# Kernel optimization log

Measured on AMD Instinct MI355X. Metric: run time of the kernel, lower is better.

The kernel has to match this reference:

```python
import jax, jax.numpy as jnp
import numpy as np

B, T, C, H = 2, 64, 384, 768
LR, MOM, DECAY = 0.01, 0.9, 0.001


def pscan(gates, tokens):
    """parallel_scan_log: x[t] = gates[t]*x[t-1] + tokens[t] along axis 1.
    gates [B,S], tokens [B,S,...]."""
    extra = tokens.ndim - gates.ndim
    g = gates.reshape(gates.shape + (1,) * extra)
    g = jnp.clip(g, 1e-7, 1.0 - 1e-7)
    lc = jnp.cumsum(jnp.log(g), axis=1)              # log cumulative gates
    return jnp.exp(lc) * jnp.cumsum(tokens * jnp.exp(-lc), axis=1)


def setup_inputs():
    key = jax.random.key(0)
    ks = jax.random.split(key, 12)
    s = 0.02
    W0 = jax.random.normal(ks[0], (H, C), jnp.float32) * s
    W1 = jax.random.normal(ks[1], (C, H), jnp.float32) * s
    return {
        "x": jax.random.normal(ks[2], (B, T, C), jnp.float32),
        "Wq": jax.random.normal(ks[3], (C, C), jnp.float32) * s, "bq": jnp.zeros((C,), jnp.float32),
        "Wk": jax.random.normal(ks[4], (C, C), jnp.float32) * s, "bk": jnp.zeros((C,), jnp.float32),
        "Wv": jax.random.normal(ks[5], (C, C), jnp.float32) * s, "bv": jnp.zeros((C,), jnp.float32),
        "Wo": jax.random.normal(ks[6], (C, C), jnp.float32) * s, "bo": jnp.zeros((C,), jnp.float32),
        "init_query": jax.random.normal(ks[7], (1, 1, C), jnp.float32) * s,
        "sW0": jnp.broadcast_to(W0, (B, H, C)) + 0.0,
        "sb0": jnp.zeros((B, H), jnp.float32),
        "sW1": jnp.broadcast_to(W1, (B, C, H)) + 0.0,
        "sb1": jnp.zeros((B, C), jnp.float32),
    }


def reference(x, Wq, bq, Wk, bk, Wv, bv, Wo, bo, init_query, sW0, sb0, sW1, sb1):
    dt = x.dtype
    # ---- retrieval (causal: uses init_query since no previous segment) ----
    q = jnp.broadcast_to(init_query, (B, 1, C)) @ Wq.T + bq          # [B,1,C]
    h_pre = jnp.einsum('bqc,bhc->bqh', q, sW0) + sb0[:, None]
    h = h_pre * jax.nn.sigmoid(h_pre)                                 # SiLU
    pred = jnp.einsum('bqh,bch->bqc', h, sW1) + sb1[:, None]
    out = pred @ Wo.T + bo                                            # [B,1,C]

    # ---- test-time memory update: per-token MSE gradients ----
    k = x @ Wk.T + bk                                                 # [B,T,C]
    v = x @ Wv.T + bv
    h1_pre = jnp.einsum('btc,bhc->bth', k, sW0) + sb0[:, None]
    sig = jax.nn.sigmoid(h1_pre)
    h1 = h1_pre * sig
    p = jnp.einsum('bth,bch->btc', h1, sW1) + sb1[:, None]
    dp = p - v                                                        # d(MSE)/d(pred)
    dW1 = jnp.einsum('btc,bth->btch', dp, h1)                         # [B,T,C,H]
    db1 = dp
    dh1 = jnp.einsum('btc,bch->bth', dp, sW1)
    dh1p = dh1 * (sig * (1 + h1_pre * (1 - sig)))                     # SiLU grad
    dW0 = jnp.einsum('bth,btc->bthc', dh1p, k)                        # [B,T,H,C]
    db0 = dh1p

    # ---- momentum scan + decayed weight scan ----
    def update(W, g):
        surprise = -LR * g                                            # [B,T,...]
        m = pscan(jnp.full((B, T), MOM, dt), (1.0 - MOM) * surprise)  # EMA of surprises
        toks = jnp.concatenate([W[:, None], m], axis=1)               # seed with current weight
        gts = jnp.concatenate([jnp.ones((B, 1), dt),
                               jnp.full((B, T), 1.0 - DECAY, dt)], axis=1)
        return pscan(gts, toks)[:, -1]                                # final weight after segment

    nW0 = update(sW0, dW0)
    nb0 = update(sb0, db0)
    nW1 = update(sW1, dW1)
    nb1 = update(sb1, db1)
    return out, nW0, nb0, nW1, nb1
```

## Files before the change

### kernel.cpp

```cpp
#include <hip/hip_runtime.h>
#include <hip/hip_bf16.h>
#include <cmath>

#define BB 2
#define TT 64
#define CC 384
#define HH 768

#define O_OUT 0
#define O_NW0 768
#define O_NB0 (768 + 589824)
#define O_NW1 (O_NB0 + 1536)
#define O_NB1 (O_NW1 + 589824)

struct Coefs { float ct[TT]; float dfac; };

typedef __attribute__((ext_vector_type(8))) short bf16x8;
typedef __attribute__((ext_vector_type(4))) float f32x4;

__device__ __forceinline__ float bf2f(unsigned short u) {
    union { unsigned int i; float f; } x; x.i = ((unsigned int)u) << 16; return x.f;
}
__device__ __forceinline__ unsigned short f2bf(float f) {
    union { float f; unsigned int i; } u; u.f = f;
    unsigned int x = u.i;
    unsigned int r = (x + 0x7fffu + ((x >> 16) & 1u)) >> 16;
    return (unsigned short)r;
}
__device__ __forceinline__ f32x4 mfma16(bf16x8 a, bf16x8 b, f32x4 c) {
    return __builtin_amdgcn_mfma_f32_16x16x32_bf16(a, b, c, 0, 0, 0);
}
__device__ __forceinline__ bf16x8 ldbf8(const unsigned short* p) {
    return *(const bf16x8*)p;
}

__global__ void k_conv(const float* __restrict__ x,  const float* __restrict__ Wq,
                       const float* __restrict__ Wk, const float* __restrict__ Wv,
                       const float* __restrict__ Wo, const float* __restrict__ sW0,
                       const float* __restrict__ sW1,
                       unsigned short* __restrict__ x_bf,  unsigned short* __restrict__ Wq_bf,
                       unsigned short* __restrict__ Wk_bf, unsigned short* __restrict__ Wv_bf,
                       unsigned short* __restrict__ Wo_bf, unsigned short* __restrict__ sW0_bf,
                       unsigned short* __restrict__ sW1_bf, unsigned short* __restrict__ sW1T_bf) {
    const int blk = blockIdx.x, j = threadIdx.x;
    if (blk < 1776) {
        int g = blk * 256 + j;
        const float* src; unsigned short* dst; int off;
        if      (g < 12288)  { src = x;   dst = x_bf;   off = g; }
        else if (g < 49152)  { src = Wq;  dst = Wq_bf;  off = g - 12288; }
        else if (g < 86016)  { src = Wk;  dst = Wk_bf;  off = g - 49152; }
        else if (g < 122880) { src = Wv;  dst = Wv_bf;  off = g - 86016; }
        else if (g < 159744) { src = Wo;  dst = Wo_bf;  off = g - 122880; }
        else if (g < 307200) { src = sW0; dst = sW0_bf; off = g - 159744; }
        else                 { src = sW1; dst = sW1_bf; off = g - 307200; }
        float4 v = ((const float4*)src)[off];
        ushort4 u;
        u.x = f2bf(v.x); u.y = f2bf(v.y); u.z = f2bf(v.z); u.w = f2bf(v.w);
        ((ushort4*)dst)[off] = u;
    } else {
        __shared__ float tile[32][33];
        const int r2 = blk - 1776;
        const int b = r2 / 288, rem = r2 % 288;
        const int c0 = (rem / 24) * 32, h0 = (rem % 24) * 32;
        const int row0 = j / 32, col = j % 32;
        #pragma unroll
        for (int r = 0; r < 4; ++r) {
            int row = row0 + r * 8;
            tile[row][col] = sW1[((size_t)(b * CC + c0 + row)) * HH + h0 + col];
        }
        __syncthreads();
        #pragma unroll
        for (int r = 0; r < 4; ++r) {
            int row = row0 + r * 8;
            sW1T_bf[((size_t)(b * HH + h0 + row)) * CC + c0 + col] = f2bf(tile[col][row]);
        }
    }
}

__global__ void k_qkv(const unsigned short* __restrict__ x_bf,
                      const unsigned short* __restrict__ Wk_bf, const float* __restrict__ bk,
                      const unsigned short* __restrict__ Wv_bf, const float* __restrict__ bv,
                      const unsigned short* __restrict__ Wq_bf, const float* __restrict__ bq,
                      const float* __restrict__ iq,
                      unsigned short* __restrict__ kb_bf, float* __restrict__ vb,
                      float* __restrict__ qb) {
    __shared__ float vecs[CC];
    __shared__ float part[16][17];
    const int blk = blockIdx.x, j = threadIdx.x;
    if (blk < 24) {
        const int wid = j >> 6, L = j & 63;
        const int w = blk * 4 + wid;
        const int mp = w % 4, np = w / 4;
        const int lrow = L & 15, kq = (L >> 4) * 8;
        const unsigned short* A0 = x_bf + (size_t)(mp * 32 + lrow) * CC;
        const unsigned short* A1 = A0 + 16 * CC;
        const int n0 = (2 * np) * 16 + lrow, n1 = n0 + 16;
        const unsigned short* B0 = (n0 < CC) ? (Wk_bf + (size_t)n0 * CC) : (Wv_bf + (size_t)(n0 - CC) * CC);
        const unsigned short* B1 = (n1 < CC) ? (Wk_bf + (size_t)n1 * CC) : (Wv_bf + (size_t)(n1 - CC) * CC);
        f32x4 acc00 = {0,0,0,0}, acc01 = {0,0,0,0}, acc10 = {0,0,0,0}, acc11 = {0,0,0,0};
        for (int s = 0; s < CC / 32; ++s) {
            int k = s * 32 + kq;
            bf16x8 a0 = ldbf8(A0 + k), a1 = ldbf8(A1 + k);
            bf16x8 b0 = ldbf8(B0 + k), b1 = ldbf8(B1 + k);
            acc00 = mfma16(a0, b0, acc00); acc01 = mfma16(a0, b1, acc01);
            acc10 = mfma16(a1, b0, acc10); acc11 = mfma16(a1, b1, acc11);
        }
        const int quad = L >> 4;
        #pragma unroll
        for (int mi = 0; mi < 2; ++mi) {
            #pragma unroll
            for (int ni = 0; ni < 2; ++ni) {
                f32x4 acc = mi == 0 ? (ni == 0 ? acc00 : acc01) : (ni == 0 ? acc10 : acc11);
                int n = (2 * np + ni) * 16 + lrow;
                #pragma unroll
                for (int r = 0; r < 4; ++r) {
                    int m = mp * 32 + mi * 16 + quad * 4 + r;
                    float v = acc[r];
                    if (n < CC) kb_bf[(size_t)m * CC + n] = f2bf(v + bk[n]);
                    else        vb[(size_t)m * CC + (n - CC)] = v + bv[n - CC];
                }
            }
        }
    } else {
        if (j < CC / 4) ((float4*)vecs)[j] = ((const float4*)iq)[j];
        __syncthreads();
        const int nt = blk - 24;
        const int nl = j & 15, ks = j >> 4;
        const int n = nt * 16 + nl;
        const unsigned short* wr = Wq_bf + (size_t)n * CC + ks * 24;
        float s = 0.f;
        for (int i = 0; i < 3; ++i) {
            bf16x8 wv8 = ldbf8(wr + i * 8);
            #pragma unroll
            for (int e = 0; e < 8; ++e)
                s += bf2f((unsigned short)wv8[e]) * vecs[ks * 24 + i * 8 + e];
        }
        part[ks][nl] = s;
        __syncthreads();
        if (j < 16) {
            float acc = bq[nt * 16 + j];
            #pragma unroll
            for (int kk = 0; kk < 16; ++kk) acc += part[kk][j];
            qb[nt * 16 + j] = acc;
        }
    }
}

__global__ void k_h1(const unsigned short* __restrict__ kb_bf, const float* __restrict__ qb,
                     const unsigned short* __restrict__ sW0_bf, const float* __restrict__ sb0,
                     unsigned short* __restrict__ h1_bf, float* __restrict__ dsil,
                     float* __restrict__ hret) {
    __shared__ float vecs[CC];
    __shared__ float part[16][17];
    const int blk = blockIdx.x, j = threadIdx.x;
    if (blk < 24) {
        const int b = blk / 12;
        const int wid = j >> 6, L = j & 63;
        const int w = (blk % 12) * 4 + wid;
        const int mp = w & 1, np = w >> 1;
        const int lrow = L & 15, kq = (L >> 4) * 8;
        const unsigned short* A0 = kb_bf + (size_t)(b * TT + mp * 32 + lrow) * CC;
        const unsigned short* A1 = A0 + 16 * CC;
        const int n0 = (2 * np) * 16 + lrow;
        const unsigned short* B0 = sW0_bf + (size_t)(b * HH + n0) * CC;
        const unsigned short* B1 = B0 + 16 * CC;
        f32x4 acc00 = {0,0,0,0}, acc01 = {0,0,0,0}, acc10 = {0,0,0,0}, acc11 = {0,0,0,0};
        for (int s = 0; s < CC / 32; ++s) {
            int k = s * 32 + kq;
            bf16x8 a0 = ldbf8(A0 + k), a1 = ldbf8(A1 + k);
            bf16x8 b0 = ldbf8(B0 + k), b1 = ldbf8(B1 + k);
            acc00 = mfma16(a0, b0, acc00); acc01 = mfma16(a0, b1, acc01);
            acc10 = mfma16(a1, b0, acc10); acc11 = mfma16(a1, b1, acc11);
        }
        const int quad = L >> 4;
        #pragma unroll
        for (int mi = 0; mi < 2; ++mi) {
            #pragma unroll
            for (int ni = 0; ni < 2; ++ni) {
                f32x4 acc = mi == 0 ? (ni == 0 ? acc00 : acc01) : (ni == 0 ? acc10 : acc11);
                int n = (2 * np + ni) * 16 + lrow;
                float bias = sb0[b * HH + n];
                #pragma unroll
                for (int r = 0; r < 4; ++r) {
                    int t = mp * 32 + mi * 16 + quad * 4 + r;
                    float pre = acc[r] + bias;
                    float sig = 1.f / (1.f + expf(-pre));
                    size_t idx = (size_t)(b * TT + t) * HH + n;
                    h1_bf[idx] = f2bf(pre * sig);
                    dsil[idx]  = sig * (1.f + pre * (1.f - sig));
                }
            }
        }
    } else {
        if (j < CC / 4) ((float4*)vecs)[j] = ((const float4*)qb)[j];
        __syncthreads();
        const int rb = blk - 24;
        const int b = rb / 48, nt = rb % 48;
        const int nl = j & 15, ks = j >> 4;
        const int n = nt * 16 + nl;
        const unsigned short* wr = sW0_bf + (size_t)(b * HH + n) * CC + ks * 24;
        float s = 0.f;
        for (int i = 0; i < 3; ++i) {
            bf16x8 wv8 = ldbf8(wr + i * 8);
            #pragma unroll
            for (int e = 0; e < 8; ++e)
                s += bf2f((unsigned short)wv8[e]) * vecs[ks * 24 + i * 8 + e];
        }
        part[ks][nl] = s;
        __syncthreads();
        if (j < 16) {
            int n2 = nt * 16 + j;
            float pre = sb0[b * HH + n2];
            #pragma unroll
            for (int kk = 0; kk < 16; ++kk) pre += part[kk][j];
            float sig = 1.f / (1.f + expf(-pre));
            hret[b * HH + n2] = pre * sig;
        }
    }
}

__global__ void k_p(const unsigned short* __restrict__ h1_bf, const float* __restrict__ hret,
                    const float* __restrict__ vb,
                    const unsigned short* __restrict__ sW1_bf, const float* __restrict__ sb1,
                    unsigned short* __restrict__ dp_bf, float* __restrict__ pred) {
    __shared__ float vecs[HH];
    __shared__ float part[16][17];
    const int blk = blockIdx.x, j = threadIdx.x;
    if (blk < 12) {
        const int b = blk / 6;
        const int wid = j >> 6, L = j & 63;
        const int w = (blk % 6) * 4 + wid;
        const int mp = w & 1, np = w >> 1;
        const int lrow = L & 15, kq = (L >> 4) * 8;
        const unsigned short* A0 = h1_bf + (size_t)(b * TT + mp * 32 + lrow) * HH;
        const unsigned short* A1 = A0 + 16 * HH;
        const int n0 = (2 * np) * 16 + lrow;
        const unsigned short* B0 = sW1_bf + (size_t)(b * CC + n0) * HH;
        const unsigned short* B1 = B0 + 16 * HH;
        f32x4 acc00 = {0,0,0,0}, acc01 = {0,0,0,0}, acc10 = {0,0,0,0}, acc11 = {0,0,0,0};
        for (int s = 0; s < HH / 32; ++s) {
            int k = s * 32 + kq;
            bf16x8 a0 = ldbf8(A0 + k), a1 = ldbf8(A1 + k);
            bf16x8 b0 = ldbf8(B0 + k), b1 = ldbf8(B1 + k);
            acc00 = mfma16(a0, b0, acc00); acc01 = mfma16(a0, b1, acc01);
            acc10 = mfma16(a1, b0, acc10); acc11 = mfma16(a1, b1, acc11);
        }
        const int quad = L >> 4;
        #pragma unroll
        for (int mi = 0; mi < 2; ++mi) {
            #pragma unroll
            for (int ni = 0; ni < 2; ++ni) {
                f32x4 acc = mi == 0 ? (ni == 0 ? acc00 : acc01) : (ni == 0 ? acc10 : acc11);
                int n = (2 * np + ni) * 16 + lrow;
                float bias = sb1[b * CC + n];
                #pragma unroll
                for (int r = 0; r < 4; ++r) {
                    int t = mp * 32 + mi * 16 + quad * 4 + r;
                    size_t idx = (size_t)(b * TT + t) * CC + n;
                    dp_bf[idx] = f2bf(acc[r] + bias - vb[idx]);
                }
            }
        }
    } else {
        const int rb = blk - 12;
        const int b = rb / 24, nt = rb % 24;
        if (j < HH / 4) ((float4*)vecs)[j] = ((const float4*)(hret + b * HH))[j];
        __syncthreads();
        const int nl = j & 15, ks = j >> 4;
        const int n = nt * 16 + nl;
        const unsigned short* wr = sW1_bf + (size_t)(b * CC + n) * HH + ks * 48;
        float s = 0.f;
        for (int i = 0; i < 6; ++i) {
            bf16x8 wv8 = ldbf8(wr + i * 8);
            #pragma unroll
            for (int e = 0; e < 8; ++e)
                s += bf2f((unsigned short)wv8[e]) * vecs[ks * 48 + i * 8 + e];
        }
        part[ks][nl] = s;
        __syncthreads();
        if (j < 16) {
            int n2 = nt * 16 + j;
            float acc = sb1[b * CC + n2];
            #pragma unroll
            for (int kk = 0; kk < 16; ++kk) acc += part[kk][j];
            pred[b * CC + n2] = acc;
        }
    }
}

__global__ void k_dh1(const unsigned short* __restrict__ dp_bf,
                      const unsigned short* __restrict__ sW1T_bf,
                      const float* __restrict__ dsil,
                      unsigned short* __restrict__ dh1p_bf) {
    const int blk = blockIdx.x, j = threadIdx.x;
    const int b = blk / 12;
    const int wid = j >> 6, L = j & 63;
    const int w = (blk % 12) * 4 + wid;
    const int mp = w & 1, np = w >> 1;
    const int lrow = L & 15, kq = (L >> 4) * 8;
    const unsigned short* A0 = dp_bf + (size_t)(b * TT + mp * 32 + lrow) * CC;
    const unsigned short* A1 = A0 + 16 * CC;
    const int n0 = (2 * np) * 16 + lrow;
    const unsigned short* B0 = sW1T_bf + (size_t)(b * HH + n0) * CC;
    const unsigned short* B1 = B0 + 16 * CC;
    f32x4 acc00 = {0,0,0,0}, acc01 = {0,0,0,0}, acc10 = {0,0,0,0}, acc11 = {0,0,0,0};
    for (int s = 0; s < CC / 32; ++s) {
        int k = s * 32 + kq;
        bf16x8 a0 = ldbf8(A0 + k), a1 = ldbf8(A1 + k);
        bf16x8 b0 = ldbf8(B0 + k), b1 = ldbf8(B1 + k);
        acc00 = mfma16(a0, b0, acc00); acc01 = mfma16(a0, b1, acc01);
        acc10 = mfma16(a1, b0, acc10); acc11 = mfma16(a1, b1, acc11);
    }
    const int quad = L >> 4;
    #pragma unroll
    for (int mi = 0; mi < 2; ++mi) {
        #pragma unroll
        for (int ni = 0; ni < 2; ++ni) {
            f32x4 acc = mi == 0 ? (ni == 0 ? acc00 : acc01) : (ni == 0 ? acc10 : acc11);
            int n = (2 * np + ni) * 16 + lrow;
            #pragma unroll
            for (int r = 0; r < 4; ++r) {
                int t = mp * 32 + mi * 16 + quad * 4 + r;
                size_t idx = (size_t)(b * TT + t) * HH + n;
                dh1p_bf[idx] = f2bf(acc[r] * dsil[idx]);
            }
        }
    }
}

__global__ void k_epi(const unsigned short* __restrict__ dp_bf,
                      const unsigned short* __restrict__ h1_bf,
                      const unsigned short* __restrict__ dh1p_bf,
                      const unsigned short* __restrict__ kb_bf,
                      const float* __restrict__ pred,
                      const float* __restrict__ sW0, const float* __restrict__ sb0,
                      const float* __restrict__ sW1, const float* __restrict__ sb1,
                      const unsigned short* __restrict__ Wo_bf, const float* __restrict__ bo,
                      float* __restrict__ out, Coefs cf) {
    __shared__ float a_t[TT][32];
    __shared__ float e_t[TT][64];
    __shared__ float vecs[CC];
    __shared__ float part[16][17];
    const int blk = blockIdx.x, j = threadIdx.x;

    if (blk < 288) {
        const int b = blk / 144, rem = blk % 144;
        const int c0 = (rem / 12) * 32, h0 = (rem % 12) * 64;
        for (int i = j; i < TT * 32; i += 256) {
            int t = i >> 5, c = i & 31;
            a_t[t][c] = cf.ct[t] * bf2f(dp_bf[((size_t)(b * TT + t)) * CC + c0 + c]);
        }
        for (int i = j; i < TT * 64; i += 256) {
            int t = i >> 6, h = i & 63;
            e_t[t][h] = bf2f(h1_bf[((size_t)(b * TT + t)) * HH + h0 + h]);
        }
        __syncthreads();
        const int ci = j & 31, hb = (j >> 5) * 8;
        float acc[8] = {0, 0, 0, 0, 0, 0, 0, 0};
        for (int t = 0; t < TT; ++t) {
            float av = a_t[t][ci];
            #pragma unroll
            for (int m = 0; m < 8; ++m) acc[m] += av * e_t[t][hb + m];
        }
        const size_t idx = ((size_t)b * CC + c0 + ci) * HH + h0 + hb;
        const float4* w4 = (const float4*)(sW1 + idx);
        float4 wa = w4[0], wb = w4[1];
        float4 o0, o1;
        o0.x = cf.dfac * wa.x - acc[0]; o0.y = cf.dfac * wa.y - acc[1];
        o0.z = cf.dfac * wa.z - acc[2]; o0.w = cf.dfac * wa.w - acc[3];
        o1.x = cf.dfac * wb.x - acc[4]; o1.y = cf.dfac * wb.y - acc[5];
        o1.z = cf.dfac * wb.z - acc[6]; o1.w = cf.dfac * wb.w - acc[7];
        *(float4*)(out + O_NW1 + idx) = o0;
        *(float4*)(out + O_NW1 + idx + 4) = o1;
    } else if (blk < 576) {
        const int bk2 = blk - 288;
        const int b = bk2 / 144, rem = bk2 % 144;
        const int h0 = (rem / 6) * 32, c0 = (rem % 6) * 64;
        for (int i = j; i < TT * 32; i += 256) {
            int t = i >> 5, h = i & 31;
            a_t[t][h] = cf.ct[t] * bf2f(dh1p_bf[((size_t)(b * TT + t)) * HH + h0 + h]);
        }
        for (int i = j; i < TT * 64; i += 256) {
            int t = i >> 6, c = i & 63;
            e_t[t][c] = bf2f(kb_bf[((size_t)(b * TT + t)) * CC + c0 + c]);
        }
        __syncthreads();
        const int hi = j & 31, cb = (j >> 5) * 8;
        float acc[8] = {0, 0, 0, 0, 0, 0, 0, 0};
        for (int t = 0; t < TT; ++t) {
            float av = a_t[t][hi];
            #pragma unroll
            for (int m = 0; m < 8; ++m) acc[m] += av * e_t[t][cb + m];
        }
        const size_t idx = ((size_t)b * HH + h0 + hi) * CC + c0 + cb;
        const float4* w4 = (const float4*)(sW0 + idx);
        float4 wa = w4[0], wb = w4[1];
        float4 o0, o1;
        o0.x = cf.dfac * wa.x - acc[0]; o0.y = cf.dfac * wa.y - acc[1];
        o0.z = cf.dfac * wa.z - acc[2]; o0.w = cf.dfac * wa.w - acc[3];
        o1.x = cf.dfac * wb.x - acc[4]; o1.y = cf.dfac * wb.y - acc[5];
        o1.z = cf.dfac * wb.z - acc[6]; o1.w = cf.dfac * wb.w - acc[7];
        *(float4*)(out + O_NW0 + idx) = o0;
        *(float4*)(out + O_NW0 + idx + 4) = o1;
    } else if (blk < 624) {
        const int rb = blk - 576;
        const int b = rb / 24, nt = rb % 24;
        if (j < CC / 4) ((float4*)vecs)[j] = ((const float4*)(pred + b * CC))[j];
        __syncthreads();
        const int nl = j & 15, ks = j >> 4;
        const int n = nt * 16 + nl;
        const unsigned short* wr = Wo_bf + (size_t)n * CC + ks * 24;
        float s = 0.f;
        for (int i = 0; i < 3; ++i) {
            bf16x8 wv8 = ldbf8(wr + i * 8);
            #pragma unroll
            for (int e = 0; e < 8; ++e)
                s += bf2f((unsigned short)wv8[e]) * vecs[ks * 24 + i * 8 + e];
        }
        part[ks][nl] = s;
        __syncthreads();
        if (j < 16) {
            int n2 = nt * 16 + j;
            float acc = bo[n2];
            #pragma unroll
            for (int kk = 0; kk < 16; ++kk) acc += part[kk][j];
            out[O_OUT + b * CC + n2] = acc;
        }
    } else {
        const int b = blk - 624;
        for (int c = j; c < CC; c += 256) {
            float acc = 0.f;
            for (int t = 0; t < TT; ++t)
                acc += cf.ct[t] * bf2f(dp_bf[((size_t)(b * TT + t)) * CC + c]);
            out[O_NB1 + b * CC + c] = cf.dfac * sb1[b * CC + c] - acc;
        }
        for (int h = j; h < HH; h += 256) {
            float acc = 0.f;
            for (int t = 0; t < TT; ++t)
                acc += cf.ct[t] * bf2f(dh1p_bf[((size_t)(b * TT + t)) * HH + h]);
            out[O_NB0 + b * HH + h] = cf.dfac * sb0[b * HH + h] - acc;
        }
    }
}

extern "C" void kernel_launch(void* const* d_in, const int* in_sizes, int n_in,
                              void* d_out, int out_size, void* d_ws, size_t ws_size,
                              hipStream_t stream) {
    const float* x   = (const float*)d_in[0];
    const float* Wq  = (const float*)d_in[1];
    const float* bq  = (const float*)d_in[2];
    const float* Wk  = (const float*)d_in[3];
    const float* bk  = (const float*)d_in[4];
    const float* Wv  = (const float*)d_in[5];
    const float* bv  = (const float*)d_in[6];
    const float* Wo  = (const float*)d_in[7];
    const float* bo  = (const float*)d_in[8];
    const float* iq  = (const float*)d_in[9];
    const float* sW0 = (const float*)d_in[10];
    const float* sb0 = (const float*)d_in[11];
    const float* sW1 = (const float*)d_in[12];
    const float* sb1 = (const float*)d_in[13];

    float* fw = (float*)d_ws;
    float* qb   = fw;
    float* hret = qb + 384;
    float* pred = hret + 1536;
    float* vb   = pred + 768;
    float* dsil = vb + 49152;
    unsigned short* us = (unsigned short*)(dsil + 98304);
    unsigned short* x_bf    = us;
    unsigned short* kb_bf   = x_bf + 49152;
    unsigned short* h1_bf   = kb_bf + 49152;
    unsigned short* dp_bf   = h1_bf + 98304;
    unsigned short* dh1p_bf = dp_bf + 49152;
    unsigned short* Wq_bf   = dh1p_bf + 98304;
    unsigned short* Wk_bf   = Wq_bf + 147456;
    unsigned short* Wv_bf   = Wk_bf + 147456;
    unsigned short* Wo_bf   = Wv_bf + 147456;
    unsigned short* sW0_bf  = Wo_bf + 147456;
    unsigned short* sW1_bf  = sW0_bf + 589824;
    unsigned short* sW1T_bf = sW1_bf + 589824;

    Coefs cf;
    const double mom = 0.9, decay = 1.0 - 0.001, lr = 0.01;
    for (int s = 0; s < TT; ++s) {
        double sum = 0.0;
        for (int t = s; t < TT; ++t) sum += pow(decay, (double)(TT - 1 - t)) * pow(mom, (double)(t - s));
        cf.ct[s] = (float)(lr * (1.0 - mom) * sum);
    }
    cf.dfac = (float)pow(decay, (double)TT);

    k_conv<<<dim3(1776 + 576), dim3(256), 0, stream>>>(x, Wq, Wk, Wv, Wo, sW0, sW1,
        x_bf, Wq_bf, Wk_bf, Wv_bf, Wo_bf, sW0_bf, sW1_bf, sW1T_bf);
    k_qkv<<<dim3(48), dim3(256), 0, stream>>>(x_bf, Wk_bf, bk, Wv_bf, bv, Wq_bf, bq, iq,
                                              kb_bf, vb, qb);
    k_h1 <<<dim3(120), dim3(256), 0, stream>>>(kb_bf, qb, sW0_bf, sb0, h1_bf, dsil, hret);
    k_p  <<<dim3(60), dim3(256), 0, stream>>>(h1_bf, hret, vb, sW1_bf, sb1, dp_bf, pred);
    k_dh1<<<dim3(24), dim3(256), 0, stream>>>(dp_bf, sW1T_bf, dsil, dh1p_bf);
    k_epi<<<dim3(626), dim3(256), 0, stream>>>(dp_bf, h1_bf, dh1p_bf, kb_bf, pred,
                                               sW0, sb0, sW1, sb1, Wo_bf, bo,
                                               (float*)d_out, cf);
}
```

Measured before the change: 144.6 us.

## Drop bf16 pre-conversion pass; convert fp32 operands inline and restructure epilogue kernels

Removes the standalone conversion kernel that wrote bf16 copies of all weights, including a transposed sW1. Each GEMM now loads fp32 operands directly and converts them to bf16 in registers, and the matrix-vector paths use fp32 weights. The dh1 GEMM reads sW1 with strided column loads instead of a pre-transposed copy, and is merged with the dW1, bias and output-projection work into k_epi1. The dW0 update moves to its own kernel, and the bias reductions are folded into the tile epilogues. This cuts a full pass over several MB of weights and one launch, at the cost of fp32 operand loads in the GEMMs and uncoalesced strided loads for the sW1 transpose path.

Result: no change. 145.8 us (+0.8%).

```diff
diff --git a/kernel.cpp b/kernel.cpp
--- a/kernel.cpp
+++ b/kernel.cpp
@@ -33,75 +33,45 @@
 __device__ __forceinline__ bf16x8 ldbf8(const unsigned short* p) {
     return *(const bf16x8*)p;
 }
-
-__global__ void k_conv(const float* __restrict__ x,  const float* __restrict__ Wq,
-                       const float* __restrict__ Wk, const float* __restrict__ Wv,
-                       const float* __restrict__ Wo, const float* __restrict__ sW0,
-                       const float* __restrict__ sW1,
-                       unsigned short* __restrict__ x_bf,  unsigned short* __restrict__ Wq_bf,
-                       unsigned short* __restrict__ Wk_bf, unsigned short* __restrict__ Wv_bf,
-                       unsigned short* __restrict__ Wo_bf, unsigned short* __restrict__ sW0_bf,
-                       unsigned short* __restrict__ sW1_bf, unsigned short* __restrict__ sW1T_bf) {
-    const int blk = blockIdx.x, j = threadIdx.x;
-    if (blk < 1776) {
-        int g = blk * 256 + j;
-        const float* src; unsigned short* dst; int off;
-        if      (g < 12288)  { src = x;   dst = x_bf;   off = g; }
-        else if (g < 49152)  { src = Wq;  dst = Wq_bf;  off = g - 12288; }
-        else if (g < 86016)  { src = Wk;  dst = Wk_bf;  off = g - 49152; }
-        else if (g < 122880) { src = Wv;  dst = Wv_bf;  off = g - 86016; }
-        else if (g < 159744) { src = Wo;  dst = Wo_bf;  off = g - 122880; }
-        else if (g < 307200) { src = sW0; dst = sW0_bf; off = g - 159744; }
-        else                 { src = sW1; dst = sW1_bf; off = g - 307200; }
-        float4 v = ((const float4*)src)[off];
-        ushort4 u;
-        u.x = f2bf(v.x); u.y = f2bf(v.y); u.z = f2bf(v.z); u.w = f2bf(v.w);
-        ((ushort4*)dst)[off] = u;
-    } else {
-        __shared__ float tile[32][33];
-        const int r2 = blk - 1776;
-        const int b = r2 / 288, rem = r2 % 288;
-        const int c0 = (rem / 24) * 32, h0 = (rem % 24) * 32;
-        const int row0 = j / 32, col = j % 32;
-        #pragma unroll
-        for (int r = 0; r < 4; ++r) {
-            int row = row0 + r * 8;
-            tile[row][col] = sW1[((size_t)(b * CC + c0 + row)) * HH + h0 + col];
-        }
-        __syncthreads();
-        #pragma unroll
-        for (int r = 0; r < 4; ++r) {
-            int row = row0 + r * 8;
-            sW1T_bf[((size_t)(b * HH + h0 + row)) * CC + c0 + col] = f2bf(tile[col][row]);
-        }
-    }
-}
-
-__global__ void k_qkv(const unsigned short* __restrict__ x_bf,
-                      const unsigned short* __restrict__ Wk_bf, const float* __restrict__ bk,
-                      const unsigned short* __restrict__ Wv_bf, const float* __restrict__ bv,
-                      const unsigned short* __restrict__ Wq_bf, const float* __restrict__ bq,
+__device__ __forceinline__ bf16x8 ldcvt8(const float* p) {
+    float4 a = *(const float4*)p, b = *(const float4*)(p + 4);
+    bf16x8 r;
+    r[0] = (short)f2bf(a.x); r[1] = (short)f2bf(a.y); r[2] = (short)f2bf(a.z); r[3] = (short)f2bf(a.w);
+    r[4] = (short)f2bf(b.x); r[5] = (short)f2bf(b.y); r[6] = (short)f2bf(b.z); r[7] = (short)f2bf(b.w);
+    return r;
+}
+__device__ __forceinline__ bf16x8 ldcvt8s(const float* p, int stride) {
+    bf16x8 r;
+    #pragma unroll
+    for (int i = 0; i < 8; ++i) r[i] = (short)f2bf(p[(size_t)i * stride]);
+    return r;
+}
+
+__global__ void k_qkv(const float* __restrict__ x,
+                      const float* __restrict__ Wk, const float* __restrict__ bk,
+                      const float* __restrict__ Wv, const float* __restrict__ bv,
+                      const float* __restrict__ Wq, const float* __restrict__ bq,
                       const float* __restrict__ iq,
                       unsigned short* __restrict__ kb_bf, float* __restrict__ vb,
                       float* __restrict__ qb) {
-    __shared__ float vecs[CC];
-    __shared__ float part[16][17];
+    __shared__ float smem[1024 + 16 * 17];
     const int blk = blockIdx.x, j = threadIdx.x;
     if (blk < 24) {
         const int wid = j >> 6, L = j & 63;
         const int w = blk * 4 + wid;
         const int mp = w % 4, np = w / 4;
         const int lrow = L & 15, kq = (L >> 4) * 8;
-        const unsigned short* A0 = x_bf + (size_t)(mp * 32 + lrow) * CC;
-        const unsigned short* A1 = A0 + 16 * CC;
+        const float* A0 = x + (size_t)(mp * 32 + lrow) * CC;
+        const float* A1 = A0 + 16 * CC;
         const int n0 = (2 * np) * 16 + lrow, n1 = n0 + 16;
-        const unsigned short* B0 = (n0 < CC) ? (Wk_bf + (size_t)n0 * CC) : (Wv_bf + (size_t)(n0 - CC) * CC);
-        const unsigned short* B1 = (n1 < CC) ? (Wk_bf + (size_t)n1 * CC) : (Wv_bf + (size_t)(n1 - CC) * CC);
+        const float* B0 = (n0 < CC) ? (Wk + (size_t)n0 * CC) : (Wv + (size_t)(n0 - CC) * CC);
+        const float* B1 = (n1 < CC) ? (Wk + (size_t)n1 * CC) : (Wv + (size_t)(n1 - CC) * CC);
         f32x4 acc00 = {0,0,0,0}, acc01 = {0,0,0,0}, acc10 = {0,0,0,0}, acc11 = {0,0,0,0};
+        #pragma unroll 2
         for (int s = 0; s < CC / 32; ++s) {
             int k = s * 32 + kq;
-            bf16x8 a0 = ldbf8(A0 + k), a1 = ldbf8(A1 + k);
-            bf16x8 b0 = ldbf8(B0 + k), b1 = ldbf8(B1 + k);
+            bf16x8 a0 = ldcvt8(A0 + k), a1 = ldcvt8(A1 + k);
+            bf16x8 b0 = ldcvt8(B0 + k), b1 = ldcvt8(B1 + k);
             acc00 = mfma16(a0, b0, acc00); acc01 = mfma16(a0, b1, acc01);
             acc10 = mfma16(a1, b0, acc10); acc11 = mfma16(a1, b1, acc11);
         }
@@ -122,36 +92,35 @@
             }
         }
     } else {
-        if (j < CC / 4) ((float4*)vecs)[j] = ((const float4*)iq)[j];
+        if (j < CC / 4) ((float4*)smem)[j] = ((const float4*)iq)[j];
         __syncthreads();
         const int nt = blk - 24;
         const int nl = j & 15, ks = j >> 4;
         const int n = nt * 16 + nl;
-        const unsigned short* wr = Wq_bf + (size_t)n * CC + ks * 24;
+        const float4* wr = (const float4*)(Wq + (size_t)n * CC + ks * 24);
         float s = 0.f;
-        for (int i = 0; i < 3; ++i) {
-            bf16x8 wv8 = ldbf8(wr + i * 8);
-            #pragma unroll
-            for (int e = 0; e < 8; ++e)
-                s += bf2f((unsigned short)wv8[e]) * vecs[ks * 24 + i * 8 + e];
-        }
-        part[ks][nl] = s;
+        #pragma unroll
+        for (int i = 0; i < 6; ++i) {
+            float4 a = wr[i];
+            const float* v = smem + ks * 24 + i * 4;
+            s += a.x * v[0] + a.y * v[1] + a.z * v[2] + a.w * v[3];
+        }
+        smem[1024 + ks * 17 + nl] = s;
         __syncthreads();
         if (j < 16) {
             float acc = bq[nt * 16 + j];
             #pragma unroll
-            for (int kk = 0; kk < 16; ++kk) acc += part[kk][j];
+            for (int kk = 0; kk < 16; ++kk) acc += smem[1024 + kk * 17 + j];
             qb[nt * 16 + j] = acc;
         }
     }
 }
 
 __global__ void k_h1(const unsigned short* __restrict__ kb_bf, const float* __restrict__ qb,
-                     const unsigned short* __restrict__ sW0_bf, const float* __restrict__ sb0,
+                     const float* __restrict__ sW0, const float* __restrict__ sb0,
                      unsigned short* __restrict__ h1_bf, float* __restrict__ dsil,
                      float* __restrict__ hret) {
-    __shared__ float vecs[CC];
-    __shared__ float part[16][17];
+    __shared__ float smem[1024 + 16 * 17];
     const int blk = blockIdx.x, j = threadIdx.x;
     if (blk < 24) {
         const int b = blk / 12;
@@ -162,13 +131,14 @@
         const unsigned short* A0 = kb_bf + (size_t)(b * TT + mp * 32 + lrow) * CC;
         const unsigned short* A1 = A0 + 16 * CC;
         const int n0 = (2 * np) * 16 + lrow;
-        const unsigned short* B0 = sW0_bf + (size_t)(b * HH + n0) * CC;
-        const unsigned short* B1 = B0 + 16 * CC;
+        const float* B0 = sW0 + (size_t)(b * HH + n0) * CC;
+        const float* B1 = B0 + 16 * CC;
         f32x4 acc00 = {0,0,0,0}, acc01 = {0,0,0,0}, acc10 = {0,0,0,0}, acc11 = {0,0,0,0};
+        #pragma unroll 2
         for (int s = 0; s < CC / 32; ++s) {
             int k = s * 32 + kq;
             bf16x8 a0 = ldbf8(A0 + k), a1 = ldbf8(A1 + k);
-            bf16x8 b0 = ldbf8(B0 + k), b1 = ldbf8(B1 + k);
+            bf16x8 b0 = ldcvt8(B0 + k), b1 = ldcvt8(B1 + k);
             acc00 = mfma16(a0, b0, acc00); acc01 = mfma16(a0, b1, acc01);
             acc10 = mfma16(a1, b0, acc10); acc11 = mfma16(a1, b1, acc11);
         }
@@ -192,27 +162,27 @@
             }
         }
     } else {
-        if (j < CC / 4) ((float4*)vecs)[j] = ((const float4*)qb)[j];
+        if (j < CC / 4) ((float4*)smem)[j] = ((const float4*)qb)[j];
         __syncthreads();
         const int rb = blk - 24;
         const int b = rb / 48, nt = rb % 48;
         const int nl = j & 15, ks = j >> 4;
         const int n = nt * 16 + nl;
-        const unsigned short* wr = sW0_bf + (size_t)(b * HH + n) * CC + ks * 24;
+        const float4* wr = (const float4*)(sW0 + (size_t)(b * HH + n) * CC + ks * 24);
         float s = 0.f;
-        for (int i = 0; i < 3; ++i) {
-            bf16x8 wv8 = ldbf8(wr + i * 8);
-            #pragma unroll
-            for (int e = 0; e < 8; ++e)
-                s += bf2f((unsigned short)wv8[e]) * vecs[ks * 24 + i * 8 + e];
-        }
-        part[ks][nl] = s;
+        #pragma unroll
+        for (int i = 0; i < 6; ++i) {
+            float4 a = wr[i];
+            const float* v = smem + ks * 24 + i * 4;
+            s += a.x * v[0] + a.y * v[1] + a.z * v[2] + a.w * v[3];
+        }
+        smem[1024 + ks * 17 + nl] = s;
         __syncthreads();
         if (j < 16) {
             int n2 = nt * 16 + j;
             float pre = sb0[b * HH + n2];
             #pragma unroll
-            for (int kk = 0; kk < 16; ++kk) pre += part[kk][j];
+            for (int kk = 0; kk < 16; ++kk) pre += smem[1024 + kk * 17 + j];
             float sig = 1.f / (1.f + expf(-pre));
             hret[b * HH + n2] = pre * sig;
         }
@@ -221,10 +191,9 @@
 
 __global__ void k_p(const unsigned short* __restrict__ h1_bf, const float* __restrict__ hret,
                     const float* __restrict__ vb,
-                    const unsigned short* __restrict__ sW1_bf, const float* __restrict__ sb1,
+                    const float* __restrict__ sW1, const float* __restrict__ sb1,
                     unsigned short* __restrict__ dp_bf, float* __restrict__ pred) {
-    __shared__ float vecs[HH];
-    __shared__ float part[16][17];
+    __shared__ float smem[1024 + 16 * 17];
     const int blk = blockIdx.x, j = threadIdx.x;
     if (blk < 12) {
         const int b = blk / 6;
@@ -235,13 +204,14 @@
         const unsigned short* A0 = h1_bf + (size_t)(b * TT + mp * 32 + lrow) * HH;
         const unsigned short* A1 = A0 + 16 * HH;
         const int n0 = (2 * np) * 16 + lrow;
-        const unsigned short* B0 = sW1_bf + (size_t)(b * CC + n0) * HH;
-        const unsigned short* B1 = B0 + 16 * HH;
+        const float* B0 = sW1 + (size_t)(b * CC + n0) * HH;
+        const float* B1 = B0 + 16 * HH;
         f32x4 acc00 = {0,0,0,0}, acc01 = {0,0,0,0}, acc10 = {0,0,0,0}, acc11 = {0,0,0,0};
+        #pragma unroll 2
         for (int s = 0; s < HH / 32; ++s) {
             int k = s * 32 + kq;
             bf16x8 a0 = ldbf8(A0 + k), a1 = ldbf8(A1 + k);
-            bf16x8 b0 = ldbf8(B0 + k), b1 = ldbf8(B1 + k);
+            bf16x8 b0 = ldcvt8(B0 + k), b1 = ldcvt8(B1 + k);
             acc00 = mfma16(a0, b0, acc00); acc01 = mfma16(a0, b1, acc01);
             acc10 = mfma16(a1, b0, acc10); acc11 = mfma16(a1, b1, acc11);
         }
@@ -264,103 +234,95 @@
     } else {
         const int rb = blk - 12;
         const int b = rb / 24, nt = rb % 24;
-        if (j < HH / 4) ((float4*)vecs)[j] = ((const float4*)(hret + b * HH))[j];
+        if (j < HH / 4) ((float4*)smem)[j] = ((const float4*)(hret + b * HH))[j];
         __syncthreads();
         const int nl = j & 15, ks = j >> 4;
         const int n = nt * 16 + nl;
-        const unsigned short* wr = sW1_bf + (size_t)(b * CC + n) * HH + ks * 48;
+        const float4* wr = (const float4*)(sW1 + (size_t)(b * CC + n) * HH + ks * 48);
         float s = 0.f;
-        for (int i = 0; i < 6; ++i) {
-            bf16x8 wv8 = ldbf8(wr + i * 8);
-            #pragma unroll
-            for (int e = 0; e < 8; ++e)
-                s += bf2f((unsigned short)wv8[e]) * vecs[ks * 48 + i * 8 + e];
-        }
-        part[ks][nl] = s;
+        #pragma unroll
+        for (int i = 0; i < 12; ++i) {
+            float4 a = wr[i];
+            const float* v = smem + ks * 48 + i * 4;
+            s += a.x * v[0] + a.y * v[1] + a.z * v[2] + a.w * v[3];
+        }
+        smem[1024 + ks * 17 + nl] = s;
         __syncthreads();
         if (j < 16) {
             int n2 = nt * 16 + j;
             float acc = sb1[b * CC + n2];
             #pragma unroll
-            for (int kk = 0; kk < 16; ++kk) acc += part[kk][j];
+            for (int kk = 0; kk < 16; ++kk) acc += smem[1024 + kk * 17 + j];
             pred[b * CC + n2] = acc;
         }
     }
 }
 
-__global__ void k_dh1(const unsigned short* __restrict__ dp_bf,
-                      const unsigned short* __restrict__ sW1T_bf,
-                      const float* __restrict__ dsil,
-                      unsigned short* __restrict__ dh1p_bf) {
+__global__ void k_epi1(const unsigned short* __restrict__ dp_bf,
+                       const unsigned short* __restrict__ h1_bf,
+                       const float* __restrict__ dsil,
+                       const float* __restrict__ sW1, const float* __restrict__ sb1,
+                       const float* __restrict__ pred,
+                       const float* __restrict__ Wo, const float* __restrict__ bo,
+                       unsigned short* __restrict__ dh1p_bf,
+                       float* __restrict__ out, Coefs cf) {
+    __shared__ float smem[6144];
     const int blk = blockIdx.x, j = threadIdx.x;
-    const int b = blk / 12;
-    const int wid = j >> 6, L = j & 63;
-    const int w = (blk % 12) * 4 + wid;
-    const int mp = w & 1, np = w >> 1;
-    const int lrow = L & 15, kq = (L >> 4) * 8;
-    const unsigned short* A0 = dp_bf + (size_t)(b * TT + mp * 32 + lrow) * CC;
-    const unsigned short* A1 = A0 + 16 * CC;
-    const int n0 = (2 * np) * 16 + lrow;
-    const unsigned short* B0 = sW1T_bf + (size_t)(b * HH + n0) * CC;
-    const unsigned short* B1 = B0 + 16 * CC;
-    f32x4 acc00 = {0,0,0,0}, acc01 = {0,0,0,0}, acc10 = {0,0,0,0}, acc11 = {0,0,0,0};
-    for (int s = 0; s < CC / 32; ++s) {
-        int k = s * 32 + kq;
-        bf16x8 a0 = ldbf8(A0 + k), a1 = ldbf8(A1 + k);
-        bf16x8 b0 = ldbf8(B0 + k), b1 = ldbf8(B1 + k);
-        acc00 = mfma16(a0, b0, acc00); acc01 = mfma16(a0, b1, acc01);
-        acc10 = mfma16(a1, b0, acc10); acc11 = mfma16(a1, b1, acc11);
-    }
-    const int quad = L >> 4;
-    #pragma unroll
-    for (int mi = 0; mi < 2; ++mi) {
-        #pragma unroll
-        for (int ni = 0; ni < 2; ++ni) {
-            f32x4 acc = mi == 0 ? (ni == 0 ? acc00 : acc01) : (ni == 0 ? acc10 : acc11);
-            int n = (2 * np + ni) * 16 + lrow;
-            #pragma unroll
-            for (int r = 0; r < 4; ++r) {
-                int t = mp * 32 + mi * 16 + quad * 4 + r;
-                size_t idx = (size_t)(b * TT + t) * HH + n;
-                dh1p_bf[idx] = f2bf(acc[r] * dsil[idx]);
+    if (blk < 24) {
+        const int b = blk / 12;
+        const int wid = j >> 6, L = j & 63;
+        const int w = (blk % 12) * 4 + wid;
+        const int mp = w & 1, np = w >> 1;
+        const int lrow = L & 15, kq = (L >> 4) * 8;
+        const unsigned short* A0 = dp_bf + (size_t)(b * TT + mp * 32 + lrow) * CC;
+        const unsigned short* A1 = A0 + 16 * CC;
+        const int n0 = (2 * np) * 16 + lrow, n1 = n0 + 16;
+        const float* Bb = sW1 + (size_t)b * CC * HH;
+        f32x4 acc00 = {0,0,0,0}, acc01 = {0,0,0,0}, acc10 = {0,0,0,0}, acc11 = {0,0,0,0};
+        for (int s = 0; s < CC / 32; ++s) {
+            int k = s * 32 + kq;
+            bf16x8 a0 = ldbf8(A0 + k), a1 = ldbf8(A1 + k);
+            bf16x8 b0 = ldcvt8s(Bb + (size_t)k * HH + n0, HH);
+            bf16x8 b1 = ldcvt8s(Bb + (size_t)k * HH + n1, HH);
+            acc00 = mfma16(a0, b0, acc00); acc01 = mfma16(a0, b1, acc01);
+            acc10 = mfma16(a1, b0, acc10); acc11 = mfma16(a1, b1, acc11);
+        }
+        const int quad = L >> 4;
+        #pragma unroll
+        for (int mi = 0; mi < 2; ++mi) {
+            #pragma unroll
+            for (int ni = 0; ni < 2; ++ni) {
+                f32x4 acc = mi == 0 ? (ni == 0 ? acc00 : acc01) : (ni == 0 ? acc10 : acc11);
+                int n = (2 * np + ni) * 16 + lrow;
+                #pragma unroll
+                for (int r = 0; r < 4; ++r) {
+                    int t = mp * 32 + mi * 16 + quad * 4 + r;
+                    size_t idx = (size_t)(b * TT + t) * HH + n;
+                    dh1p_bf[idx] = f2bf(acc[r] * dsil[idx]);
+                }
             }
         }
-    }
-}
-
-__global__ void k_epi(const unsigned short* __restrict__ dp_bf,
-                      const unsigned short* __restrict__ h1_bf,
-                      const unsigned short* __restrict__ dh1p_bf,
-                      const unsigned short* __restrict__ kb_bf,
-                      const float* __restrict__ pred,
-                      const float* __restrict__ sW0, const float* __restrict__ sb0,
-                      const float* __restrict__ sW1, const float* __restrict__ sb1,
-                      const unsigned short* __restrict__ Wo_bf, const float* __restrict__ bo,
-                      float* __restrict__ out, Coefs cf) {
-    __shared__ float a_t[TT][32];
-    __shared__ float e_t[TT][64];
-    __shared__ float vecs[CC];
-    __shared__ float part[16][17];
-    const int blk = blockIdx.x, j = threadIdx.x;
-
-    if (blk < 288) {
-        const int b = blk / 144, rem = blk % 144;
+    } else if (blk < 312) {
+        float* a_t = smem;
+        float* e_t = smem + 2048;
+        const int u = blk - 24;
+        const int b = u / 144, rem = u % 144;
         const int c0 = (rem / 12) * 32, h0 = (rem % 12) * 64;
         for (int i = j; i < TT * 32; i += 256) {
             int t = i >> 5, c = i & 31;
-            a_t[t][c] = cf.ct[t] * bf2f(dp_bf[((size_t)(b * TT + t)) * CC + c0 + c]);
+            a_t[t * 32 + c] = cf.ct[t] * bf2f(dp_bf[((size_t)(b * TT + t)) * CC + c0 + c]);
         }
         for (int i = j; i < TT * 64; i += 256) {
             int t = i >> 6, h = i & 63;
-            e_t[t][h] = bf2f(h1_bf[((size_t)(b * TT + t)) * HH + h0 + h]);
+            e_t[t * 64 + h] = bf2f(h1_bf[((size_t)(b * TT + t)) * HH + h0 + h]);
         }
         __syncthreads();
         const int ci = j & 31, hb = (j >> 5) * 8;
         float acc[8] = {0, 0, 0, 0, 0, 0, 0, 0};
         for (int t = 0; t < TT; ++t) {
-            float av = a_t[t][ci];
-            #pragma unroll
-            for (int m = 0; m < 8; ++m) acc[m] += av * e_t[t][hb + m];
+            float av = a_t[t * 32 + ci];
+            #pragma unroll
+            for (int m = 0; m < 8; ++m) acc[m] += av * e_t[t * 64 + hb + m];
         }
         const size_t idx = ((size_t)b * CC + c0 + ci) * HH + h0 + hb;
         const float4* w4 = (const float4*)(sW1 + idx);
@@ -372,74 +334,78 @@
         o1.z = cf.dfac * wb.z - acc[6]; o1.w = cf.dfac * wb.w - acc[7];
         *(float4*)(out + O_NW1 + idx) = o0;
         *(float4*)(out + O_NW1 + idx + 4) = o1;
-    } else if (blk < 576) {
-        const int bk2 = blk - 288;
-        const int b = bk2 / 144, rem = bk2 % 144;
-        const int h0 = (rem / 6) * 32, c0 = (rem % 6) * 64;
-        for (int i = j; i < TT * 32; i += 256) {
-            int t = i >> 5, h = i & 31;
-            a_t[t][h] = cf.ct[t] * bf2f(dh1p_bf[((size_t)(b * TT + t)) * HH + h0 + h]);
-        }
-        for (int i = j; i < TT * 64; i += 256) {
-            int t = i >> 6, c = i & 63;
-            e_t[t][c] = bf2f(kb_bf[((size_t)(b * TT + t)) * CC + c0 + c]);
-        }
-        __syncthreads();
-        const int hi = j & 31, cb = (j >> 5) * 8;
-        float acc[8] = {0, 0, 0, 0, 0, 0, 0, 0};
-        for (int t = 0; t < TT; ++t) {
-            float av = a_t[t][hi];
-            #pragma unroll
-            for (int m = 0; m < 8; ++m) acc[m] += av * e_t[t][cb + m];
-        }
-        const size_t idx = ((size_t)b * HH + h0 + hi) * CC + c0 + cb;
-        const float4* w4 = (const float4*)(sW0 + idx);
-        float4 wa = w4[0], wb = w4[1];
-        float4 o0, o1;
-        o0.x = cf.dfac * wa.x - acc[0]; o0.y = cf.dfac * wa.y - acc[1];
-        o0.z = cf.dfac * wa.z - acc[2]; o0.w = cf.dfac * wa.w - acc[3];
-        o1.x = cf.dfac * wb.x - acc[4]; o1.y = cf.dfac * wb.y - acc[5];
-        o1.z = cf.dfac * wb.z - acc[6]; o1.w = cf.dfac * wb.w - acc[7];
-        *(float4*)(out + O_NW0 + idx) = o0;
-        *(float4*)(out + O_NW0 + idx + 4) = o1;
-    } else if (blk < 624) {
-        const int rb = blk - 576;
+        if (h0 == 0 && j < 32) {
+            float s = 0.f;
+            for (int t = 0; t < TT; ++t) s += a_t[t * 32 + j];
+            out[O_NB1 + b * CC + c0 + j] = cf.dfac * sb1[b * CC + c0 + j] - s;
+        }
+    } else {
+        const int rb = blk - 312;
         const int b = rb / 24, nt = rb % 24;
-        if (j < CC / 4) ((float4*)vecs)[j] = ((const float4*)(pred + b * CC))[j];
+        if (j < CC / 4) ((float4*)smem)[j] = ((const float4*)(pred + b * CC))[j];
         __syncthreads();
         const int nl = j & 15, ks = j >> 4;
         const int n = nt * 16 + nl;
-        const unsigned short* wr = Wo_bf + (size_t)n * CC + ks * 24;
+        const float4* wr = (const float4*)(Wo + (size_t)n * CC + ks * 24);
         float s = 0.f;
-        for (int i = 0; i < 3; ++i) {
-            bf16x8 wv8 = ldbf8(wr + i * 8);
-            #pragma unroll
-            for (int e = 0; e < 8; ++e)
-                s += bf2f((unsigned short)wv8[e]) * vecs[ks * 24 + i * 8 + e];
-        }
-        part[ks][nl] = s;
+        #pragma unroll
+        for (int i = 0; i < 6; ++i) {
+            float4 a = wr[i];
+            const float* v = smem + ks * 24 + i * 4;
+            s += a.x * v[0] + a.y * v[1] + a.z * v[2] + a.w * v[3];
+        }
+        smem[1024 + ks * 17 + nl] = s;
         __syncthreads();
         if (j < 16) {
             int n2 = nt * 16 + j;
             float acc = bo[n2];
             #pragma unroll
-            for (int kk = 0; kk < 16; ++kk) acc += part[kk][j];
+            for (int kk = 0; kk < 16; ++kk) acc += smem[1024 + kk * 17 + j];
             out[O_OUT + b * CC + n2] = acc;
         }
-    } else {
-        const int b = blk - 624;
-        for (int c = j; c < CC; c += 256) {
-            float acc = 0.f;
-            for (int t = 0; t < TT; ++t)
-                acc += cf.ct[t] * bf2f(dp_bf[((size_t)(b * TT + t)) * CC + c]);
-            out[O_NB1 + b * CC + c] = cf.dfac * sb1[b * CC + c] - acc;
-        }
-        for (int h = j; h < HH; h += 256) {
-            float acc = 0.f;
-            for (int t = 0; t < TT; ++t)
-                acc += cf.ct[t] * bf2f(dh1p_bf[((size_t)(b * TT + t)) * HH + h]);
-            out[O_NB0 + b * HH + h] = cf.dfac * sb0[b * HH + h] - acc;
-        }
+    }
+}
+
+__global__ void k_epi2(const unsigned short* __restrict__ dh1p_bf,
+                       const unsigned short* __restrict__ kb_bf,
+                       const float* __restrict__ sW0, const float* __restrict__ sb0,
+                       float* __restrict__ out, Coefs cf) {
+    __shared__ float smem[6144];
+    float* a_t = smem;
+    float* e_t = smem + 2048;
+    const int blk = blockIdx.x, j = threadIdx.x;
+    const int b = blk / 144, rem = blk % 144;
+    const int h0 = (rem / 6) * 32, c0 = (rem % 6) * 64;
+    for (int i = j; i < TT * 32; i += 256) {
+        int t = i >> 5, h = i & 31;
+        a_t[t * 32 + h] = cf.ct[t] * bf2f(dh1p_bf[((size_t)(b * TT + t)) * HH + h0 + h]);
+    }
+    for (int i = j; i < TT * 64; i += 256) {
+        int t = i >> 6, c = i & 63;
+        e_t[t * 64 + c] = bf2f(kb_bf[((size_t)(b * TT + t)) * CC + c0 + c]);
+    }
+    __syncthreads();
+    const int hi = j & 31, cb = (j >> 5) * 8;
+    float acc[8] = {0, 0, 0, 0, 0, 0, 0, 0};
+    for (int t = 0; t < TT; ++t) {
+        float av = a_t[t * 32 + hi];
+        #pragma unroll
+        for (int m = 0; m < 8; ++m) acc[m] += av * e_t[t * 64 + cb + m];
+    }
+    const size_t idx = ((size_t)b * HH + h0 + hi) * CC + c0 + cb;
+    const float4* w4 = (const float4*)(sW0 + idx);
+    float4 wa = w4[0], wb = w4[1];
+    float4 o0, o1;
+    o0.x = cf.dfac * wa.x - acc[0]; o0.y = cf.dfac * wa.y - acc[1];
+    o0.z = cf.dfac * wa.z - acc[2]; o0.w = cf.dfac * wa.w - acc[3];
+    o1.x = cf.dfac * wb.x - acc[4]; o1.y = cf.dfac * wb.y - acc[5];
+    o1.z = cf.dfac * wb.z - acc[6]; o1.w = cf.dfac * wb.w - acc[7];
+    *(float4*)(out + O_NW0 + idx) = o0;
+    *(float4*)(out + O_NW0 + idx + 4) = o1;
+    if (c0 == 0 && j < 32) {
+        float s = 0.f;
+        for (int t = 0; t < TT; ++t) s += a_t[t * 32 + j];
+        out[O_NB0 + b * HH + h0 + j] = cf.dfac * sb0[b * HH + h0 + j] - s;
     }
 }
 
@@ -468,18 +434,10 @@
     float* vb   = pred + 768;
     float* dsil = vb + 49152;
     unsigned short* us = (unsigned short*)(dsil + 98304);
-    unsigned short* x_bf    = us;
-    unsigned short* kb_bf   = x_bf + 49152;
+    unsigned short* kb_bf   = us;
     unsigned short* h1_bf   = kb_bf + 49152;
     unsigned short* dp_bf   = h1_bf + 98304;
     unsigned short* dh1p_bf = dp_bf + 49152;
-    unsigned short* Wq_bf   = dh1p_bf + 98304;
-    unsigned short* Wk_bf   = Wq_bf + 147456;
-    unsigned short* Wv_bf   = Wk_bf + 147456;
-    unsigned short* Wo_bf   = Wv_bf + 147456;
-    unsigned short* sW0_bf  = Wo_bf + 147456;
-    unsigned short* sW1_bf  = sW0_bf + 589824;
-    unsigned short* sW1T_bf = sW1_bf + 589824;
 
     Coefs cf;
     const double mom = 0.9, decay = 1.0 - 0.001, lr = 0.01;
@@ -490,14 +448,10 @@
     }
     cf.dfac = (float)pow(decay, (double)TT);
 
-    k_conv<<<dim3(1776 + 576), dim3(256), 0, stream>>>(x, Wq, Wk, Wv, Wo, sW0, sW1,
-        x_bf, Wq_bf, Wk_bf, Wv_bf, Wo_bf, sW0_bf, sW1_bf, sW1T_bf);
-    k_qkv<<<dim3(48), dim3(256), 0, stream>>>(x_bf, Wk_bf, bk, Wv_bf, bv, Wq_bf, bq, iq,
-                                              kb_bf, vb, qb);
-    k_h1 <<<dim3(120), dim3(256), 0, stream>>>(kb_bf, qb, sW0_bf, sb0, h1_bf, dsil, hret);
-    k_p  <<<dim3(60), dim3(256), 0, stream>>>(h1_bf, hret, vb, sW1_bf, sb1, dp_bf, pred);
-    k_dh1<<<dim3(24), dim3(256), 0, stream>>>(dp_bf, sW1T_bf, dsil, dh1p_bf);
-    k_epi<<<dim3(626), dim3(256), 0, stream>>>(dp_bf, h1_bf, dh1p_bf, kb_bf, pred,
-                                               sW0, sb0, sW1, sb1, Wo_bf, bo,
-                                               (float*)d_out, cf);
-}
+    k_qkv <<<dim3(48),  dim3(256), 0, stream>>>(x, Wk, bk, Wv, bv, Wq, bq, iq, kb_bf, vb, qb);
+    k_h1  <<<dim3(120), dim3(256), 0, stream>>>(kb_bf, qb, sW0, sb0, h1_bf, dsil, hret);
+    k_p   <<<dim3(60),  dim3(256), 0, stream>>>(h1_bf, hret, vb, sW1, sb1, dp_bf, pred);
+    k_epi1<<<dim3(360), dim3(256), 0, stream>>>(dp_bf, h1_bf, dsil, sW1, sb1, pred, Wo, bo,
+                                                dh1p_bf, (float*)d_out, cf);
+    k_epi2<<<dim3(288), dim3(256), 0, stream>>>(dh1p_bf, kb_bf, sW0, sb0, (float*)d_out, cf);
+}
```
